# Optimization experiments

Hardware: AMD Instinct MI355X
Metric: run time of the kernel (lower is better)

## Reference

```python
import jax, jax.numpy as jnp
import numpy as np

N, E, R = 30000, 480000, 8192
N_IN, E_IN = 128, 64
N_HID, E_HID = 256, 128
N_OUT, E_OUT = 256, 64
N_CLASS, N_COL = 10, 128
NEG = 0.01  # LeakyReLU slope


def leaky(x):
    return jnp.where(x > 0, x, NEG * x)


def pe_init(n_pos, d):
    # sinusoid position encoding table (position_encoding_init)
    pe = np.array([[p / np.power(10000, 2 * (j // 2) / d) for j in range(d)]
                   if p != 0 else np.zeros(d) for p in range(n_pos)])
    pe[1:, 0::2] = np.sin(pe[1:, 0::2])
    pe[1:, 1::2] = np.cos(pe[1:, 1::2])
    return jnp.asarray(pe, jnp.float32)


def segment_mean(vals, idx, n):
    s = jax.ops.segment_sum(vals, idx, num_segments=n)
    c = jax.ops.segment_sum(jnp.ones((vals.shape[0], 1), vals.dtype), idx, num_segments=n)
    return s / jnp.maximum(c, 1.0)


def esage(x, e, src, dst, We, be, Wn, bn):
    # edge update from [x_src ; e], mean-aggregate messages to dst nodes, node update
    e2 = leaky(jnp.concatenate([x[src], e], axis=-1) @ We + be)      # [E, e_out]
    h = segment_mean(e2, dst, x.shape[0])                             # [N, e_out]
    x2 = leaky(jnp.concatenate([x, h], axis=-1) @ Wn + bn)            # [N, n_out]
    return x2, e2


def setup_inputs():
    key = jax.random.key(0)
    ks = jax.random.split(key, 24)

    def xav(k, shp):
        std = float(np.sqrt(2.0 / (shp[0] + shp[1])))
        return jax.random.normal(k, shp, jnp.float32) * std

    return {
        'x': jax.random.normal(ks[0], (N, N_IN), jnp.float32),
        'e': jax.random.normal(ks[1], (E, E_IN), jnp.float32),
        'src': jax.random.randint(ks[2], (E,), 0, N),
        'dst': jax.random.randint(ks[3], (E,), 0, N),
        'row_idx': jax.random.randint(ks[4], (R,), 0, N),
        'col_idx': jax.random.randint(ks[5], (N_COL,), 0, N),
        'real': jax.random.normal(ks[6], (R * N_COL, E_OUT), jnp.float32),
        'mask': jax.random.randint(ks[7], (R, N_COL), 0, 2) == 1,
        'W1e': xav(ks[8], (N_IN + E_IN, E_HID)), 'b1e': jnp.zeros((E_HID,), jnp.float32),
        'W1n': xav(ks[9], (N_IN + E_HID, N_HID)), 'b1n': jnp.zeros((N_HID,), jnp.float32),
        'W2e': xav(ks[10], (N_HID + E_HID, E_OUT)), 'b2e': jnp.zeros((E_OUT,), jnp.float32),
        'W2n': xav(ks[11], (N_HID + E_OUT, N_OUT)), 'b2n': jnp.zeros((N_OUT,), jnp.float32),
        'node_pe': pe_init(N_COL, N_HID),
        'Wq': xav(ks[12], (N_HID, N_HID)),
        'Wk': xav(ks[13], (N_HID, N_HID)),
        'Wv': xav(ks[14], (N_HID, N_HID)),
        'Wref': xav(ks[15], (N_HID, N_HID)), 'bref': jnp.zeros((N_HID,), jnp.float32),
        'Wr': xav(ks[16], (N_OUT, E_OUT)),
        'Wc': xav(ks[17], (N_HID, E_OUT)), 'bep': jnp.zeros((E_OUT,), jnp.float32),
        'Wcls': xav(ks[18], (N_COL * E_OUT, N_CLASS)), 'bcls': jnp.zeros((N_CLASS,), jnp.float32),
    }


def reference(x, e, src, dst, row_idx, col_idx, real, mask,
              W1e, b1e, W1n, b1n, W2e, b2e, W2n, b2n,
              node_pe, Wq, Wk, Wv, Wref, bref, Wr, Wc, bep, Wcls, bcls):
    # two ESAGE message-passing layers
    x1, e1 = esage(x, e, src, dst, W1e, b1e, W1n, b1n)
    new_col = x1[col_idx]                                  # [C, n_hidden]
    x2, e2 = esage(x1, e1, src, dst, W2e, b2e, W2n, b2n)
    new_row = x2[row_idx]                                  # [R, n_out]

    # node self-attention (hand-rolled, incl. the duplicated dist@v from the source)
    c = new_col + node_pe
    q, k, v = c @ Wq, c @ Wk, c @ Wv
    dist = jax.nn.softmax((q @ k.T) * (1.0 / np.sqrt(N_HID)), axis=-1)
    c = 2.0 * (dist @ v)                                    # mm(dist,v) + mm(dist,v)
    new_col = jax.nn.sigmoid(c @ Wref + bref)

    # edge predictor over all (row, col) pairs: [R, C, e_out]
    pred = leaky((new_row @ Wr)[:, None, :] + (new_col @ Wc)[None, :, :] + bep)
    pred_flat = pred.reshape(R * N_COL, E_OUT)

    # masked imputation: real where mask True, predicted elsewhere
    imput_e = jnp.where(mask.reshape(-1)[:, None], real, pred_flat)
    imput_e = imput_e.reshape(R, N_COL, E_OUT)

    # mlp classifier: Flatten -> Linear -> LogSoftmax
    res = jax.nn.log_softmax(imput_e.reshape(R, -1) @ Wcls + bcls, axis=-1)
    return (res, pred_flat)
```

## Files before the change

### kernel.cpp

```cpp
#include <hip/hip_runtime.h>
#include <hip/hip_bf16.h>
#include <math.h>

#define NNODES 30000
#define NEDGES 480000
#define RROWS  8192
#define NCOLS  128
#define NIN    128
#define EIN    64
#define NHID   256
#define EHID   128
#define NOUTD  256
#define EOUTD  64
#define NCLS   10
#define NB_PFX 118

typedef __attribute__((ext_vector_type(8))) unsigned short ushort8;
typedef __attribute__((ext_vector_type(8))) short bhalf8;
typedef __attribute__((ext_vector_type(4))) float floatx4;

__device__ __forceinline__ float lrelu(float v){ return v > 0.f ? v : 0.01f * v; }
__device__ __forceinline__ float4 ld4(const float* p){ return *(const float4*)p; }
__device__ __forceinline__ float4 ntld4(const float* p){
    floatx4 v = __builtin_nontemporal_load((const floatx4*)p);
    return make_float4(v.x, v.y, v.z, v.w);
}
__device__ __forceinline__ void ntst4(float* p, float4 v){
    floatx4 n = {v.x, v.y, v.z, v.w};
    __builtin_nontemporal_store(n, (floatx4*)p);
}
__device__ __forceinline__ void ntst8u(unsigned short* p, ushort8 v){
    __builtin_nontemporal_store(v, (ushort8*)p);
}
__device__ __forceinline__ unsigned short f2b(float f){
    unsigned int u = __builtin_bit_cast(unsigned int, f);
    u += 0x7fffu + ((u >> 16) & 1u);
    return (unsigned short)(u >> 16);
}
__device__ __forceinline__ float b2f(unsigned short b){
    unsigned int u = ((unsigned int)b) << 16;
    return __builtin_bit_cast(float, u);
}

#define PREP_CVT_N   1875
#define PREP_W1T_B   (PREP_CVT_N)
#define PREP_W1B_B   (PREP_W1T_B + 64)
#define PREP_W2T_B   (PREP_W1B_B + 32)
#define PREP_W2B_B   (PREP_W2T_B + 64)
#define PREP_W1N_B   (PREP_W2B_B + 32)
#define PREP_W2N_B   (PREP_W1N_B + 256)
#define PREP_HIST_B  (PREP_W2N_B + 320)
#define PREP_DET_B   (PREP_HIST_B + 1875)
#define PREP_TOTAL   (PREP_DET_B + 1)

__device__ __forceinline__ void wT_region(const float* __restrict__ W, unsigned short* __restrict__ Wt,
                                          int KOFF, int KSUB, int N, int idx){
    if (idx >= N * KSUB) return;
    int n = idx / KSUB, k = idx % KSUB;
    Wt[idx] = f2b(W[(size_t)(KOFF + k) * N + n]);
}

__global__ __launch_bounds__(256) void k_prep(
    const float* __restrict__ x, unsigned short* __restrict__ xb,
    const float* __restrict__ W1e, unsigned short* __restrict__ W1tT, unsigned short* __restrict__ W1bT,
    const float* __restrict__ W2e, unsigned short* __restrict__ W2tT, unsigned short* __restrict__ W2bT,
    const float* __restrict__ W1n, unsigned short* __restrict__ W1nTb,
    const float* __restrict__ W2n, unsigned short* __restrict__ W2nTb,
    const int* __restrict__ dst, int* __restrict__ cnt_i,
    const unsigned int* __restrict__ mask, int* __restrict__ mode)
{
    const int bid = blockIdx.x, t = threadIdx.x;
    if (bid < PREP_CVT_N){
        int i = bid * 256 + t;
        float4 a = ntld4(x + (size_t)i * 8), b = ntld4(x + (size_t)i * 8 + 4);
        ushort8 o = {f2b(a.x), f2b(a.y), f2b(a.z), f2b(a.w), f2b(b.x), f2b(b.y), f2b(b.z), f2b(b.w)};
        *(ushort8*)(xb + (size_t)i * 8) = o;
    } else if (bid < PREP_W1B_B){
        wT_region(W1e, W1tT, 0, 128, 128, (bid - PREP_W1T_B) * 256 + t);
    } else if (bid < PREP_W2T_B){
        wT_region(W1e, W1bT, 128, 64, 128, (bid - PREP_W1B_B) * 256 + t);
    } else if (bid < PREP_W2B_B){
        wT_region(W2e, W2tT, 0, 256, 64, (bid - PREP_W2T_B) * 256 + t);
    } else if (bid < PREP_W1N_B){
        wT_region(W2e, W2bT, 256, 128, 64, (bid - PREP_W2B_B) * 256 + t);
    } else if (bid < PREP_W2N_B){
        wT_region(W1n, W1nTb, 0, 256, 256, (bid - PREP_W1N_B) * 256 + t);
    } else if (bid < PREP_HIST_B){
        wT_region(W2n, W2nTb, 0, 320, 256, (bid - PREP_W2N_B) * 256 + t);
    } else if (bid < PREP_DET_B){
        int i = (bid - PREP_HIST_B) * 256 + t;
        if (i < NEDGES) atomicAdd(&cnt_i[dst[i]], 1);
    } else if (t == 0){
        bool allI32 = true, allF32 = true;
        for (int i = 0; i < 64; i++){
            unsigned int v = mask[i];
            if (!(v == 0u || v == 1u)) allI32 = false;
            if (!(v == 0u || v == 0x3F800000u)) allF32 = false;
        }
        *mode = allI32 ? 0 : (allF32 ? 1 : 2);
    }
}

__global__ __launch_bounds__(256) void k_pfx1(const int* __restrict__ cnt_i, int* __restrict__ blocksum){
    __shared__ int red[256];
    const int t = threadIdx.x;
    const int i = blockIdx.x * 256 + t;
    red[t] = (i < NNODES) ? cnt_i[i] : 0;
    __syncthreads();
    for (int o = 128; o; o >>= 1){ if (t < o) red[t] += red[t + o]; __syncthreads(); }
    if (t == 0) blocksum[blockIdx.x] = red[0];
}
__global__ __launch_bounds__(128) void k_pfx2(const int* __restrict__ blocksum, int* __restrict__ blockoff){
    __shared__ int s[128];
    const int t = threadIdx.x;
    int v = (t < NB_PFX) ? blocksum[t] : 0;
    s[t] = v;
    __syncthreads();
    for (int o = 1; o < 128; o <<= 1){
        int add = (t >= o) ? s[t - o] : 0;
        __syncthreads();
        s[t] += add;
        __syncthreads();
    }
    if (t < NB_PFX) blockoff[t] = s[t] - v;
}
__global__ __launch_bounds__(256) void k_pfx3(const int* __restrict__ cnt_i, const int* __restrict__ blockoff,
                                              int* __restrict__ cursor, float* __restrict__ cntf){
    __shared__ int s[256];
    const int t = threadIdx.x;
    const int i = blockIdx.x * 256 + t;
    int v = (i < NNODES) ? cnt_i[i] : 0;
    s[t] = v;
    __syncthreads();
    for (int o = 1; o < 256; o <<= 1){
        int add = (t >= o) ? s[t - o] : 0;
        __syncthreads();
        s[t] += add;
        __syncthreads();
    }
    if (i < NNODES){
        cursor[i] = s[t] - v + blockoff[blockIdx.x];
        cntf[i] = (float)v;
    }
}

__global__ void k_scatter(const int* __restrict__ dst, int* __restrict__ cursor, int* __restrict__ eidx){
    int i = blockIdx.x * 256 + threadIdx.x;
    if (i >= NEDGES) return;
    int pos = atomicAdd(&cursor[dst[i]], 1);
    eidx[pos] = i;
}
__global__ void k_sgather(const int* __restrict__ src, const int* __restrict__ dst,
                          const int* __restrict__ eidx,
                          int* __restrict__ srcs, int* __restrict__ dsts){
    int p = blockIdx.x * 256 + threadIdx.x;
    if (p >= NEDGES) return;
    int i = eidx[p];
    srcs[p] = src[i];
    dsts[p] = dst[i];
}

template<int K, int N>
__global__ __launch_bounds__(256) void k_gemm_b16(
    const unsigned short* __restrict__ Ab, const unsigned short* __restrict__ Wt,
    unsigned short* __restrict__ outb, int M)
{
    __shared__ unsigned short At[64][K + 8];
    const int t = threadIdx.x;
    const int r0 = blockIdx.x * 64;
    {
        const int r = t >> 2, q = t & 3;
        const int row = r0 + r;
        const bool valid = row < M;
        const unsigned short* a = Ab + (size_t)(valid ? row : 0) * K;
        for (int kk = q * (K / 4); kk < (q + 1) * (K / 4); kk += 8){
            ushort8 u;
            if (valid) u = *(const ushort8*)(a + kk);
            else       u = (ushort8){0,0,0,0,0,0,0,0};
            *(ushort8*)&At[r][kk] = u;
        }
    }
    __syncthreads();
    const int lane = t & 63, w = t >> 6;
    const int fr = lane & 15, fq = lane >> 4;
    constexpr int NF = N / 16;
    floatx4 acc[NF] = {};
    #pragma unroll
    for (int ks = 0; ks < K / 32; ks++){
        const int k = ks * 32 + fq * 8;
        bhalf8 a = *(bhalf8*)&At[w * 16 + fr][k];
        #pragma unroll
        for (int n = 0; n < NF; n++){
            bhalf8 b = *(const bhalf8*)(Wt + (size_t)(n * 16 + fr) * K + k);
            acc[n] = __builtin_amdgcn_mfma_f32_16x16x32_bf16(a, b, acc[n], 0, 0, 0);
        }
    }
    #pragma unroll
    for (int n = 0; n < NF; n++){
        const int col = n * 16 + fr;
        #pragma unroll
        for (int rr = 0; rr < 4; rr++){
            const int row = r0 + w * 16 + fq * 4 + rr;
            if (row < M) outb[(size_t)row * N + col] = f2b(acc[n][rr]);
        }
    }
}

__global__ __launch_bounds__(256) void k_edge1_fused(
    const float* __restrict__ e,
    const int* __restrict__ srcs, const int* __restrict__ dsts, const int* __restrict__ eidx,
    const unsigned short* __restrict__ W1bT, const float* __restrict__ b1e,
    const unsigned short* __restrict__ P1b, const unsigned short* __restrict__ W2bT,
    unsigned short* __restrict__ Qb, float* __restrict__ hsum)
{
    __shared__ unsigned short Cb[64][136];
    __shared__ unsigned short P1s[64][136];
    __shared__ int dstS[64];
    const int t = threadIdx.x;
    const int r = t >> 2, q = t & 3;
    const int lane = t & 63, w = t >> 6;
    const int wm = w >> 1, wn = w & 1;
    const int fr = lane & 15, fq = lane >> 4;
    const int base = blockIdx.x * 128;

    float4 f0, f1, f2, f3;
    ushort8 u0, u1, u2, u3;
    int dcur;

    {
        const int p = base + r;
        dcur = dsts[p];
        const int srow = srcs[p];
        const int ei = eidx[p];
        const float* ep = e + (size_t)ei * 64 + q * 16;
        f0 = ntld4(ep); f1 = ntld4(ep + 4); f2 = ntld4(ep + 8); f3 = ntld4(ep + 12);
        const unsigned short* pp = P1b + (size_t)srow * 128 + q * 32;
        u0 = *(const ushort8*)pp;       u1 = *(const ushort8*)(pp + 8);
        u2 = *(const ushort8*)(pp + 16); u3 = *(const ushort8*)(pp + 24);
    }

    #pragma unroll
    for (int tile = 0; tile < 2; tile++){
        const int p0 = base + tile * 64;
        if (tile) __syncthreads();
        if (q == 0) dstS[r] = dcur;
        {
            ushort8 e0 = {f2b(f0.x), f2b(f0.y), f2b(f0.z), f2b(f0.w), f2b(f1.x), f2b(f1.y), f2b(f1.z), f2b(f1.w)};
            ushort8 e1v = {f2b(f2.x), f2b(f2.y), f2b(f2.z), f2b(f2.w), f2b(f3.x), f2b(f3.y), f2b(f3.z), f2b(f3.w)};
            *(ushort8*)&Cb[r][q * 16]     = e0;
            *(ushort8*)&Cb[r][q * 16 + 8] = e1v;
            *(ushort8*)&P1s[r][q * 32]      = u0;
            *(ushort8*)&P1s[r][q * 32 + 8]  = u1;
            *(ushort8*)&P1s[r][q * 32 + 16] = u2;
            *(ushort8*)&P1s[r][q * 32 + 24] = u3;
        }
        __syncthreads();
        if (tile == 0){
            const int p = base + 64 + r;
            dcur = dsts[p];
            const int srow = srcs[p];
            const int ei = eidx[p];
            const float* ep = e + (size_t)ei * 64 + q * 16;
            f0 = ntld4(ep); f1 = ntld4(ep + 4); f2 = ntld4(ep + 8); f3 = ntld4(ep + 12);
            const unsigned short* pp = P1b + (size_t)srow * 128 + q * 32;
            u0 = *(const ushort8*)pp;       u1 = *(const ushort8*)(pp + 8);
            u2 = *(const ushort8*)(pp + 16); u3 = *(const ushort8*)(pp + 24);
        }
        floatx4 acc1[2][4] = {};
        #pragma unroll
        for (int ks = 0; ks < 2; ks++){
            const int k = ks * 32 + fq * 8;
            bhalf8 a0 = *(bhalf8*)&Cb[wm * 32 + fr][k];
            bhalf8 a1 = *(bhalf8*)&Cb[wm * 32 + 16 + fr][k];
            #pragma unroll
            for (int n = 0; n < 4; n++){
                const int col = wn * 64 + n * 16 + fr;
                bhalf8 b = *(const bhalf8*)(W1bT + (size_t)col * 64 + k);
                acc1[0][n] = __builtin_amdgcn_mfma_f32_16x16x32_bf16(a0, b, acc1[0][n], 0, 0, 0);
                acc1[1][n] = __builtin_amdgcn_mfma_f32_16x16x32_bf16(a1, b, acc1[1][n], 0, 0, 0);
            }
        }
        __syncthreads();
        #pragma unroll
        for (int m = 0; m < 2; m++){
            #pragma unroll
            for (int n = 0; n < 4; n++){
                const int col = wn * 64 + n * 16 + fr;
                const float bv = b1e[col];
                #pragma unroll
                for (int rr = 0; rr < 4; rr++){
                    const int row = wm * 32 + m * 16 + fq * 4 + rr;
                    const float pv = b2f(P1s[row][col]);
                    Cb[row][col] = f2b(lrelu(acc1[m][n][rr] + pv + bv));
                }
            }
        }
        __syncthreads();
        {
            floatx4 acc2[4] = {};
            #pragma unroll
            for (int ks = 0; ks < 4; ks++){
                const int k = ks * 32 + fq * 8;
                bhalf8 a = *(bhalf8*)&Cb[w * 16 + fr][k];
                #pragma unroll
                for (int n = 0; n < 4; n++){
                    bhalf8 b = *(const bhalf8*)(W2bT + (size_t)(n * 16 + fr) * 128 + k);
                    acc2[n] = __builtin_amdgcn_mfma_f32_16x16x32_bf16(a, b, acc2[n], 0, 0, 0);
                }
            }
            #pragma unroll
            for (int n = 0; n < 4; n++){
                const int col = n * 16 + fr;
                #pragma unroll
                for (int rr = 0; rr < 4; rr++){
                    const int row = w * 16 + fq * 4 + rr;
                    P1s[row][col] = f2b(acc2[n][rr]);
                }
            }
        }
        __syncthreads();
        {
            unsigned short* op = Qb + (size_t)(p0 + r) * 64 + q * 16;
            ntst8u(op,     *(ushort8*)&P1s[r][q * 16]);
            ntst8u(op + 8, *(ushort8*)&P1s[r][q * 16 + 8]);
        }
        {
            const int col = t & 127, half = t >> 7;
            const int rbase = half * 32;
            float s = 0.f;
            int prev = dstS[rbase];
            #pragma unroll 4
            for (int rr = 0; rr < 32; rr++){
                const int rw2 = rbase + rr;
                const int d = dstS[rw2];
                if (d != prev){
                    atomicAdd(&hsum[(size_t)prev * EHID + col], s);
                    s = 0.f; prev = d;
                }
                s += b2f(Cb[rw2][col]);
            }
            atomicAdd(&hsum[(size_t)prev * EHID + col], s);
        }
    }
}

__global__ __launch_bounds__(256) void k_edge2_lite(
    const unsigned short* __restrict__ P2b, const unsigned short* __restrict__ Qb,
    const int* __restrict__ srcs, const int* __restrict__ dsts,
    const float* __restrict__ b2e, float* __restrict__ hsum)
{
    const int t = threadIdx.x;
    const int lane = t & 63, w = t >> 6;
    const int p0 = blockIdx.x * 256 + w * 64;
    const float bias = b2e[lane];
    float s = 0.f;
    int prev = dsts[p0];
    #pragma unroll 4
    for (int i = 0; i < 64; i++){
        const int p = p0 + i;
        const int d = dsts[p];
        if (d != prev){
            atomicAdd(&hsum[(size_t)prev * EOUTD + lane], s);
            s = 0.f; prev = d;
        }
        const float q  = b2f(__builtin_nontemporal_load(&Qb[(size_t)p * 64 + lane]));
        const float pv = b2f(P2b[(size_t)srcs[p] * 64 + lane]);
        s += lrelu(pv + q + bias);
    }
    atomicAdd(&hsum[(size_t)prev * EOUTD + lane], s);
}

__global__ __launch_bounds__(256) void k_node1_p2(
    const unsigned short* __restrict__ A1b, const float* __restrict__ hsum,
    const float* __restrict__ cntf,
    const unsigned short* __restrict__ Wt, const float* __restrict__ bias,
    const unsigned short* __restrict__ W2tT,
    unsigned short* __restrict__ x1b, unsigned short* __restrict__ P2b, int M)
{
    constexpr int K = 256;
    __shared__ unsigned short At[32][K + 8];
    const int t = threadIdx.x;
    const int r0 = blockIdx.x * 32;
    {
        const int r = t >> 3, q = t & 7;
        const int row = r0 + r;
        const bool valid = row < M;
        float rinv = 0.f;
        const unsigned short* a1 = A1b;
        const float* a2 = hsum;
        if (valid){
            rinv = 1.f / fmaxf(cntf[row], 1.f);
            a1 = A1b  + (size_t)row * NIN;
            a2 = hsum + (size_t)row * EHID;
        }
        for (int kk = q * 32; kk < q * 32 + 32; kk += 8){
            ushort8 u;
            if (!valid){
                u = (ushort8){0,0,0,0,0,0,0,0};
            } else if (kk < NIN){
                u = *(const ushort8*)(a1 + kk);
            } else {
                float4 g0 = ld4(a2 + (kk - NIN)), g1 = ld4(a2 + (kk - NIN) + 4);
                u = (ushort8){f2b(g0.x*rinv), f2b(g0.y*rinv), f2b(g0.z*rinv), f2b(g0.w*rinv),
                              f2b(g1.x*rinv), f2b(g1.y*rinv), f2b(g1.z*rinv), f2b(g1.w*rinv)};
            }
            *(ushort8*)&At[r][kk] = u;
        }
    }
    __syncthreads();
    const int lane = t & 63, w = t >> 6;
    const int wm = w >> 1, wn = w & 1;
    const int fr = lane & 15, fq = lane >> 4;
    floatx4 acc[8] = {};
    #pragma unroll
    for (int ks = 0; ks < 8; ks++){
        const int k = ks * 32 + fq * 8;
        bhalf8 a = *(bhalf8*)&At[wm * 16 + fr][k];
        #pragma unroll
        for (int n = 0; n < 8; n++){
            const int col = wn * 128 + n * 16 + fr;
            bhalf8 b = *(const bhalf8*)(Wt + (size_t)col * K + k);
            acc[n] = __builtin_amdgcn_mfma_f32_16x16x32_bf16(a, b, acc[n], 0, 0, 0);
        }
    }
    __syncthreads();
    #pragma unroll
    for (int n = 0; n < 8; n++){
        const int col = wn * 128 + n * 16 + fr;
        const float bv = bias[col];
        #pragma unroll
        for (int rr = 0; rr < 4; rr++){
            const int row = r0 + wm * 16 + fq * 4 + rr;
            unsigned short ob = f2b(lrelu(acc[n][rr] + bv));
            At[wm * 16 + fq * 4 + rr][col] = ob;
            if (row < M) x1b[(size_t)row * 256 + col] = ob;
        }
    }
    __syncthreads();
    {
        floatx4 acc2[2] = {};
        #pragma unroll
        for (int ks = 0; ks < 8; ks++){
            const int k = ks * 32 + fq * 8;
            bhalf8 a = *(bhalf8*)&At[wm * 16 + fr][k];
            #pragma unroll
            for (int n = 0; n < 2; n++){
                const int col = wn * 32 + n * 16 + fr;
                bhalf8 b = *(const bhalf8*)(W2tT + (size_t)col * 256 + k);
                acc2[n] = __builtin_amdgcn_mfma_f32_16x16x32_bf16(a, b, acc2[n], 0, 0, 0);
            }
        }
        #pragma unroll
        for (int n = 0; n < 2; n++){
            const int col = wn * 32 + n * 16 + fr;
            #pragma unroll
            for (int rr = 0; rr < 4; rr++){
                const int row = r0 + wm * 16 + fq * 4 + rr;
                if (row < M) P2b[(size_t)row * 64 + col] = f2b(acc2[n][rr]);
            }
        }
    }
}

__global__ __launch_bounds__(256) void k_node2(
    const unsigned short* __restrict__ A1b, const float* __restrict__ hsum,
    const float* __restrict__ cntf,
    const unsigned short* __restrict__ Wt, const float* __restrict__ bias,
    unsigned short* __restrict__ outb, int M)
{
    constexpr int K = 320;
    __shared__ unsigned short At[32][K + 8];
    const int t = threadIdx.x;
    const int r0 = blockIdx.x * 32;
    {
        const int r = t >> 3, q = t & 7;
        const int row = r0 + r;
        const bool valid = row < M;
        float rinv = 0.f;
        const unsigned short* a1 = A1b;
        const float* a2 = hsum;
        if (valid){
            rinv = 1.f / fmaxf(cntf[row], 1.f);
            a1 = A1b  + (size_t)row * NHID;
            a2 = hsum + (size_t)row * EOUTD;
        }
        for (int kk = q * 40; kk < q * 40 + 40; kk += 8){
            ushort8 u;
            if (!valid){
                u = (ushort8){0,0,0,0,0,0,0,0};
            } else if (kk < NHID){
                u = *(const ushort8*)(a1 + kk);
            } else {
                float4 g0 = ld4(a2 + (kk - NHID)), g1 = ld4(a2 + (kk - NHID) + 4);
                u = (ushort8){f2b(g0.x*rinv), f2b(g0.y*rinv), f2b(g0.z*rinv), f2b(g0.w*rinv),
                              f2b(g1.x*rinv), f2b(g1.y*rinv), f2b(g1.z*rinv), f2b(g1.w*rinv)};
            }
            *(ushort8*)&At[r][kk] = u;
        }
    }
    __syncthreads();
    const int lane = t & 63, w = t >> 6;
    const int wm = w >> 1, wn = w & 1;
    const int fr = lane & 15, fq = lane >> 4;
    floatx4 acc[8] = {};
    #pragma unroll
    for (int ks = 0; ks < 10; ks++){
        const int k = ks * 32 + fq * 8;
        bhalf8 a = *(bhalf8*)&At[wm * 16 + fr][k];
        #pragma unroll
        for (int n = 0; n < 8; n++){
            const int col = wn * 128 + n * 16 + fr;
            bhalf8 b = *(const bhalf8*)(Wt + (size_t)col * K + k);
            acc[n] = __builtin_amdgcn_mfma_f32_16x16x32_bf16(a, b, acc[n], 0, 0, 0);
        }
    }
    #pragma unroll
    for (int n = 0; n < 8; n++){
        const int col = wn * 128 + n * 16 + fr;
        const float bv = bias[col];
        #pragma unroll
        for (int rr = 0; rr < 4; rr++){
            const int row = r0 + wm * 16 + fq * 4 + rr;
            if (row < M) outb[(size_t)row * 256 + col] = f2b(lrelu(acc[n][rr] + bv));
        }
    }
}

__global__ __launch_bounds__(256) void k_attn_qkv(
    const unsigned short* __restrict__ x1b, const int* __restrict__ col_idx,
    const float* __restrict__ pe,
    const float* __restrict__ Wq, const float* __restrict__ Wk, const float* __restrict__ Wv,
    float* __restrict__ qo, float* __restrict__ ko, float* __restrict__ vo)
{
    __shared__ float c[256];
    const int i = blockIdx.x, t = threadIdx.x;
    const int col = col_idx[i];
    c[t] = b2f(x1b[(size_t)col * 256 + t]) + pe[i * 256 + t];
    __syncthreads();
    float aq = 0.f, ak = 0.f, av = 0.f;
    #pragma unroll 4
    for (int kk = 0; kk < 256; kk++){
        float cv = c[kk];
        aq += cv * Wq[kk * 256 + t];
        ak += cv * Wk[kk * 256 + t];
        av += cv * Wv[kk * 256 + t];
    }
    qo[i * 256 + t] = aq; ko[i * 256 + t] = ak; vo[i * 256 + t] = av;
}

__global__ __launch_bounds__(128) void k_attn_dist(
    const float* __restrict__ q, const float* __restrict__ k, float* __restrict__ dist)
{
    __shared__ float qr[256];
    __shared__ float red[128];
    const int i = blockIdx.x, t = threadIdx.x;
    qr[t] = q[i * 256 + t]; qr[t + 128] = q[i * 256 + t + 128];
    __syncthreads();
    float s = 0.f;
    #pragma unroll 4
    for (int kk = 0; kk < 256; kk++) s += qr[kk] * k[t * 256 + kk];
    s *= 0.0625f;
    red[t] = s; __syncthreads();
    for (int off = 64; off; off >>= 1){ if (t < off) red[t] = fmaxf(red[t], red[t + off]); __syncthreads(); }
    float m = red[0]; __syncthreads();
    float ex = expf(s - m);
    red[t] = ex; __syncthreads();
    for (int off = 64; off; off >>= 1){ if (t < off) red[t] += red[t + off]; __syncthreads(); }
    dist[i * 128 + t] = ex / red[0];
}

__global__ __launch_bounds__(256) void k_attn_out(
    const float* __restrict__ dist, const float* __restrict__ v,
    const float* __restrict__ Wref, const float* __restrict__ bref,
    const float* __restrict__ Wc, const float* __restrict__ bep,
    float* __restrict__ colWc)
{
    __shared__ float dr[128];
    __shared__ float c2[256];
    __shared__ float nc[256];
    const int i = blockIdx.x, t = threadIdx.x;
    if (t < 128) dr[t] = dist[i * 128 + t];
    __syncthreads();
    float s = 0.f;
    #pragma unroll 4
    for (int j = 0; j < 128; j++) s += dr[j] * v[j * 256 + t];
    c2[t] = 2.f * s;
    __syncthreads();
    float a = 0.f;
    #pragma unroll 4
    for (int kk = 0; kk < 256; kk++) a += c2[kk] * Wref[kk * 256 + t];
    a += bref[t];
    nc[t] = 1.f / (1.f + expf(-a));
    __syncthreads();
    if (t < 64){
        float o = 0.f;
        #pragma unroll 4
        for (int kk = 0; kk < 256; kk++) o += nc[kk] * Wc[kk * 64 + t];
        colWc[i * 64 + t] = o + bep[t];
    }
}

__global__ __launch_bounds__(256) void k_rowwr(
    const unsigned short* __restrict__ x2b, const int* __restrict__ row_idx,
    const float* __restrict__ Wr, float* __restrict__ rw)
{
    __shared__ unsigned short A[16][264];
    const int t = threadIdx.x;
    const int r0 = blockIdx.x * 16;
    const int rl = t >> 4, cg = t & 15;
    const int ridx = row_idx[r0 + rl];
    const unsigned short* ar = x2b + (size_t)ridx * 256;
    for (int i = cg; i < 32; i += 16) *(ushort8*)&A[rl][i * 8] = *(const ushort8*)(ar + i * 8);
    __syncthreads();
    float acc[4] = {0.f, 0.f, 0.f, 0.f};
    #pragma unroll 4
    for (int kk = 0; kk < 256; kk++){
        float4 w = ld4(Wr + (size_t)kk * 64 + cg * 4);
        float a = b2f(A[rl][kk]);
        acc[0] += a * w.x; acc[1] += a * w.y; acc[2] += a * w.z; acc[3] += a * w.w;
    }
    *(float4*)(rw + (size_t)(r0 + rl) * 64 + cg * 4) = make_float4(acc[0], acc[1], acc[2], acc[3]);
}

__global__ __launch_bounds__(256) void k_pred8(
    const float* __restrict__ rowWr, const float* __restrict__ colWc,
    const void* __restrict__ maskp, const int* __restrict__ modep,
    const float* __restrict__ real, const float* __restrict__ Wcls, const float* __restrict__ bcls,
    float* __restrict__ out)
{
    __shared__ float colWc_s[8192];
    __shared__ float rowWr_s[8 * 64];
    __shared__ unsigned char mask_s[8 * 128];
    __shared__ float part[4][80];
    __shared__ float logits_s[80];
    const int t  = threadIdx.x;
    const int r0 = blockIdx.x * 8;
    const int mode = *modep;
    for (int idx = t; idx < 2048; idx += 256)
        *(float4*)&colWc_s[idx * 4] = ld4(colWc + idx * 4);
    for (int idx = t; idx < 128; idx += 256)
        *(float4*)&rowWr_s[idx * 4] = ld4(rowWr + (size_t)r0 * 64 + idx * 4);
    for (int idx = t; idx < 1024; idx += 256){
        const int g = idx >> 7, c = idx & 127;
        const int gi = (r0 + g) * 128 + c;
        bool m;
        if (mode == 2)      m = ((const unsigned char*)maskp)[gi] != 0;
        else if (mode == 0) m = ((const int*)maskp)[gi] != 0;
        else                m = ((const float*)maskp)[gi] != 0.f;
        mask_s[idx] = m ? 1 : 0;
    }
    __syncthreads();

    float acc[8][10];
    #pragma unroll
    for (int g = 0; g < 8; g++)
        #pragma unroll
        for (int c = 0; c < 10; c++) acc[g][c] = 0.f;
    float* pred = out + RROWS * NCLS;

    #pragma unroll 1
    for (int i = 0; i < 8; i++){
        const int e4   = i * 256 + t;
        const int base = e4 * 4;
        const int c = base >> 6;
        const int j = base & 63;
        float4 cw = ld4(&colWc_s[c * 64 + j]);
        float w40[40];
        #pragma unroll
        for (int u = 0; u < 10; u++){
            float4 wv = ld4(Wcls + (size_t)base * 10 + u * 4);
            w40[u*4+0] = wv.x; w40[u*4+1] = wv.y; w40[u*4+2] = wv.z; w40[u*4+3] = wv.w;
        }
        #pragma unroll
        for (int g = 0; g < 8; g++){
            const int rr = r0 + g;
            float4 rwv = ld4(&rowWr_s[g * 64 + j]);
            float4 p;
            p.x = lrelu(rwv.x + cw.x); p.y = lrelu(rwv.y + cw.y);
            p.z = lrelu(rwv.z + cw.z); p.w = lrelu(rwv.w + cw.w);
            ntst4(pred + (size_t)rr * 8192 + base, p);
            float4 im = p;
            if (mask_s[g * 128 + c]) im = ntld4(real + (size_t)rr * 8192 + base);
            #pragma unroll
            for (int cls = 0; cls < 10; cls++){
                acc[g][cls] += im.x * w40[cls]      + im.y * w40[10 + cls]
                             + im.z * w40[20 + cls] + im.w * w40[30 + cls];
            }
        }
    }
    #pragma unroll
    for (int g = 0; g < 8; g++)
        #pragma unroll
        for (int cls = 0; cls < 10; cls++){
            float v = acc[g][cls];
            for (int off = 32; off; off >>= 1) v += __shfl_down(v, off, 64);
            acc[g][cls] = v;
        }
    const int wid = t >> 6, lane = t & 63;
    if (lane == 0){
        #pragma unroll
        for (int g = 0; g < 8; g++)
            #pragma unroll
            for (int cls = 0; cls < 10; cls++) part[wid][g * 10 + cls] = acc[g][cls];
    }
    __syncthreads();
    if (t < 80) logits_s[t] = part[0][t] + part[1][t] + part[2][t] + part[3][t] + bcls[t % 10];
    __syncthreads();
    if (t < 8){
        float m = -1e30f;
        #pragma unroll
        for (int cls = 0; cls < 10; cls++) m = fmaxf(m, logits_s[t * 10 + cls]);
        float se = 0.f;
        #pragma unroll
        for (int cls = 0; cls < 10; cls++) se += expf(logits_s[t * 10 + cls] - m);
        float ls = logf(se) + m;
        #pragma unroll
        for (int cls = 0; cls < 10; cls++) out[(r0 + t) * 10 + cls] = logits_s[t * 10 + cls] - ls;
    }
}

extern "C" void kernel_launch(void* const* d_in, const int* in_sizes, int n_in,
                              void* d_out, int out_size, void* d_ws, size_t ws_size,
                              hipStream_t stream)
{
    const float* x      = (const float*)d_in[0];
    const float* e      = (const float*)d_in[1];
    const int*   src    = (const int*)d_in[2];
    const int*   dst    = (const int*)d_in[3];
    const int*   row_idx= (const int*)d_in[4];
    const int*   col_idx= (const int*)d_in[5];
    const float* real   = (const float*)d_in[6];
    const void*  mask   = d_in[7];
    const float* W1e    = (const float*)d_in[8];
    const float* b1e    = (const float*)d_in[9];
    const float* W1n    = (const float*)d_in[10];
    const float* b1n    = (const float*)d_in[11];
    const float* W2e    = (const float*)d_in[12];
    const float* b2e    = (const float*)d_in[13];
    const float* W2n    = (const float*)d_in[14];
    const float* b2n    = (const float*)d_in[15];
    const float* pe     = (const float*)d_in[16];
    const float* Wq     = (const float*)d_in[17];
    const float* Wk     = (const float*)d_in[18];
    const float* Wv     = (const float*)d_in[19];
    const float* Wref   = (const float*)d_in[20];
    const float* bref   = (const float*)d_in[21];
    const float* Wr     = (const float*)d_in[22];
    const float* Wc     = (const float*)d_in[23];
    const float* bep    = (const float*)d_in[24];
    const float* Wcls   = (const float*)d_in[25];
    const float* bcls   = (const float*)d_in[26];

    float* ws = (float*)d_ws;
    size_t off = 0;
    float* h1sum = ws + off; off += (size_t)NNODES * EHID;
    float* h2sum = ws + off; off += (size_t)NNODES * EOUTD;
    int*   cnt_i = (int*)(ws + off); off += NNODES;
    const size_t zero_floats = off;
    float* cntf  = ws + off; off += NNODES;
    int*   cursor= (int*)(ws + off); off += NNODES;
    int*   srcs  = (int*)(ws + off); off += NEDGES;
    int*   dsts  = (int*)(ws + off); off += NEDGES;
    int*   eidx  = (int*)(ws + off); off += NEDGES;
    unsigned short* xb    = (unsigned short*)(ws + off); off += (size_t)NNODES * NIN  / 2;
    unsigned short* x1b   = (unsigned short*)(ws + off); off += (size_t)NNODES * NHID / 2;
    unsigned short* x2b   = (unsigned short*)(ws + off); off += (size_t)NNODES * NOUTD / 2;
    unsigned short* W1tT  = (unsigned short*)(ws + off); off += 128 * 128 / 2;
    unsigned short* W1bT  = (unsigned short*)(ws + off); off += 128 * 64 / 2;
    unsigned short* W2tT  = (unsigned short*)(ws + off); off += 64 * 256 / 2;
    unsigned short* W2bT  = (unsigned short*)(ws + off); off += 64 * 128 / 2;
    unsigned short* W1nTb = (unsigned short*)(ws + off); off += 256 * 256 / 2;
    unsigned short* W2nTb = (unsigned short*)(ws + off); off += 256 * 320 / 2;
    unsigned short* P1b   = (unsigned short*)(ws + off); off += (size_t)NNODES * 128 / 2;
    unsigned short* P2b   = (unsigned short*)(ws + off); off += (size_t)NNODES * 64 / 2;
    float* qb    = ws + off; off += 128 * 256;
    float* kb    = ws + off; off += 128 * 256;
    float* vb    = ws + off; off += 128 * 256;
    float* distb = ws + off; off += 128 * 128;
    float* colWc = ws + off; off += 128 * 64;
    float* rowWrb= ws + off; off += (size_t)RROWS * EOUTD;
    int*   modep = (int*)(ws + off); off += 4;
    int*   blocksum = (int*)(ws + off); off += 128;
    int*   blockoff = (int*)(ws + off); off += 128;
    unsigned short* Qb;
    size_t need = (off + (size_t)NEDGES * 32) * sizeof(float);
    if (ws_size >= need) Qb = (unsigned short*)(ws + off);
    else                 Qb = (unsigned short*)((float*)d_out + (size_t)RROWS * NCLS);

    (void)hipMemsetAsync(d_ws, 0, zero_floats * sizeof(float), stream);
    k_prep<<<PREP_TOTAL, 256, 0, stream>>>(x, xb, W1e, W1tT, W1bT, W2e, W2tT, W2bT,
                                           W1n, W1nTb, W2n, W2nTb, dst, cnt_i,
                                           (const unsigned int*)mask, modep);
    k_pfx1<<<NB_PFX, 256, 0, stream>>>(cnt_i, blocksum);
    k_pfx2<<<1, 128, 0, stream>>>(blocksum, blockoff);
    k_pfx3<<<NB_PFX, 256, 0, stream>>>(cnt_i, blockoff, cursor, cntf);
    k_scatter<<<(NEDGES + 255) / 256, 256, 0, stream>>>(dst, cursor, eidx);
    k_sgather<<<(NEDGES + 255) / 256, 256, 0, stream>>>(src, dst, eidx, srcs, dsts);
    k_gemm_b16<128, 128><<<(NNODES + 63) / 64, 256, 0, stream>>>(xb, W1tT, P1b, NNODES);
    k_edge1_fused<<<NEDGES / 128, 256, 0, stream>>>(e, srcs, dsts, eidx, W1bT, b1e, P1b, W2bT, Qb, h1sum);
    k_node1_p2<<<(NNODES + 31) / 32, 256, 0, stream>>>(xb, h1sum, cntf, W1nTb, b1n, W2tT, x1b, P2b, NNODES);
    k_edge2_lite<<<NEDGES / 256, 256, 0, stream>>>(P2b, Qb, srcs, dsts, b2e, h2sum);
    k_node2<<<(NNODES + 31) / 32, 256, 0, stream>>>(x1b, h2sum, cntf, W2nTb, b2n, x2b, NNODES);
    k_attn_qkv<<<128, 256, 0, stream>>>(x1b, col_idx, pe, Wq, Wk, Wv, qb, kb, vb);
    k_attn_dist<<<128, 128, 0, stream>>>(qb, kb, distb);
    k_attn_out<<<128, 256, 0, stream>>>(distb, vb, Wref, bref, Wc, bep, colWc);
    k_rowwr<<<RROWS / 16, 256, 0, stream>>>(x2b, row_idx, Wr, rowWrb);
    k_pred8<<<RROWS / 8, 256, 0, stream>>>(rowWrb, colWc, mask, modep, real, Wcls, bcls, (float*)d_out);
}
```

Before: 627.1 us.

## Pre-gather edge features to sorted bf16 buffer in sgather; simplify edge1 kernel

```diff
diff --git a/kernel.cpp b/kernel.cpp
--- a/kernel.cpp
+++ b/kernel.cpp
@@ -150,14 +150,23 @@
     int pos = atomicAdd(&cursor[dst[i]], 1);
     eidx[pos] = i;
 }
-__global__ void k_sgather(const int* __restrict__ src, const int* __restrict__ dst,
-                          const int* __restrict__ eidx,
-                          int* __restrict__ srcs, int* __restrict__ dsts){
-    int p = blockIdx.x * 256 + threadIdx.x;
-    if (p >= NEDGES) return;
-    int i = eidx[p];
-    srcs[p] = src[i];
-    dsts[p] = dst[i];
+
+__global__ __launch_bounds__(256) void k_sgather(
+    const int* __restrict__ src, const int* __restrict__ dst, const int* __restrict__ eidx,
+    const float* __restrict__ e,
+    int* __restrict__ srcs, int* __restrict__ dsts, unsigned short* __restrict__ es)
+{
+    const int t = threadIdx.x;
+    const int r = t >> 2, q = t & 3;
+    const int p = blockIdx.x * 64 + r;
+    const int i = eidx[p];
+    if (q == 0){ srcs[p] = src[i]; dsts[p] = dst[i]; }
+    const float* ep = e + (size_t)i * 64 + q * 16;
+    float4 f0 = ntld4(ep), f1 = ntld4(ep + 4), f2 = ntld4(ep + 8), f3 = ntld4(ep + 12);
+    ushort8 u0 = {f2b(f0.x), f2b(f0.y), f2b(f0.z), f2b(f0.w), f2b(f1.x), f2b(f1.y), f2b(f1.z), f2b(f1.w)};
+    ushort8 u1 = {f2b(f2.x), f2b(f2.y), f2b(f2.z), f2b(f2.w), f2b(f3.x), f2b(f3.y), f2b(f3.z), f2b(f3.w)};
+    ntst8u(es + (size_t)p * 64 + q * 16,     u0);
+    ntst8u(es + (size_t)p * 64 + q * 16 + 8, u1);
 }
 
 template<int K, int N>
@@ -207,8 +216,8 @@
 }
 
 __global__ __launch_bounds__(256) void k_edge1_fused(
-    const float* __restrict__ e,
-    const int* __restrict__ srcs, const int* __restrict__ dsts, const int* __restrict__ eidx,
+    const unsigned short* __restrict__ es,
+    const int* __restrict__ srcs, const int* __restrict__ dsts,
     const unsigned short* __restrict__ W1bT, const float* __restrict__ b1e,
     const unsigned short* __restrict__ P1b, const unsigned short* __restrict__ W2bT,
     unsigned short* __restrict__ Qb, float* __restrict__ hsum)
@@ -217,130 +226,99 @@
     __shared__ unsigned short P1s[64][136];
     __shared__ int dstS[64];
     const int t = threadIdx.x;
+    const int p0 = blockIdx.x * 64;
     const int r = t >> 2, q = t & 3;
+    {
+        const int p = p0 + r;
+        if (q == 0) dstS[r] = dsts[p];
+        const int srow = srcs[p];
+        const unsigned short* pp = P1b + (size_t)srow * 128 + q * 32;
+        *(ushort8*)&P1s[r][q * 32]      = *(const ushort8*)pp;
+        *(ushort8*)&P1s[r][q * 32 + 8]  = *(const ushort8*)(pp + 8);
+        *(ushort8*)&P1s[r][q * 32 + 16] = *(const ushort8*)(pp + 16);
+        *(ushort8*)&P1s[r][q * 32 + 24] = *(const ushort8*)(pp + 24);
+        const unsigned short* ep = es + (size_t)p * 64 + q * 16;
+        *(ushort8*)&Cb[r][q * 16]     = *(const ushort8*)ep;
+        *(ushort8*)&Cb[r][q * 16 + 8] = *(const ushort8*)(ep + 8);
+    }
+    __syncthreads();
     const int lane = t & 63, w = t >> 6;
     const int wm = w >> 1, wn = w & 1;
     const int fr = lane & 15, fq = lane >> 4;
-    const int base = blockIdx.x * 128;
-
-    float4 f0, f1, f2, f3;
-    ushort8 u0, u1, u2, u3;
-    int dcur;
-
-    {
-        const int p = base + r;
-        dcur = dsts[p];
-        const int srow = srcs[p];
-        const int ei = eidx[p];
-        const float* ep = e + (size_t)ei * 64 + q * 16;
-        f0 = ntld4(ep); f1 = ntld4(ep + 4); f2 = ntld4(ep + 8); f3 = ntld4(ep + 12);
-        const unsigned short* pp = P1b + (size_t)srow * 128 + q * 32;
-        u0 = *(const ushort8*)pp;       u1 = *(const ushort8*)(pp + 8);
-        u2 = *(const ushort8*)(pp + 16); u3 = *(const ushort8*)(pp + 24);
-    }
-
-    #pragma unroll
-    for (int tile = 0; tile < 2; tile++){
-        const int p0 = base + tile * 64;
-        if (tile) __syncthreads();
-        if (q == 0) dstS[r] = dcur;
-        {
-            ushort8 e0 = {f2b(f0.x), f2b(f0.y), f2b(f0.z), f2b(f0.w), f2b(f1.x), f2b(f1.y), f2b(f1.z), f2b(f1.w)};
-            ushort8 e1v = {f2b(f2.x), f2b(f2.y), f2b(f2.z), f2b(f2.w), f2b(f3.x), f2b(f3.y), f2b(f3.z), f2b(f3.w)};
-            *(ushort8*)&Cb[r][q * 16]     = e0;
-            *(ushort8*)&Cb[r][q * 16 + 8] = e1v;
-            *(ushort8*)&P1s[r][q * 32]      = u0;
-            *(ushort8*)&P1s[r][q * 32 + 8]  = u1;
-            *(ushort8*)&P1s[r][q * 32 + 16] = u2;
-            *(ushort8*)&P1s[r][q * 32 + 24] = u3;
-        }
-        __syncthreads();
-        if (tile == 0){
-            const int p = base + 64 + r;
-            dcur = dsts[p];
-            const int srow = srcs[p];
-            const int ei = eidx[p];
-            const float* ep = e + (size_t)ei * 64 + q * 16;
-            f0 = ntld4(ep); f1 = ntld4(ep + 4); f2 = ntld4(ep + 8); f3 = ntld4(ep + 12);
-            const unsigned short* pp = P1b + (size_t)srow * 128 + q * 32;
-            u0 = *(const ushort8*)pp;       u1 = *(const ushort8*)(pp + 8);
-            u2 = *(const ushort8*)(pp + 16); u3 = *(const ushort8*)(pp + 24);
-        }
-        floatx4 acc1[2][4] = {};
-        #pragma unroll
-        for (int ks = 0; ks < 2; ks++){
+    floatx4 acc1[2][4] = {};
+    #pragma unroll
+    for (int ks = 0; ks < 2; ks++){
+        const int k = ks * 32 + fq * 8;
+        bhalf8 a0 = *(bhalf8*)&Cb[wm * 32 + fr][k];
+        bhalf8 a1 = *(bhalf8*)&Cb[wm * 32 + 16 + fr][k];
+        #pragma unroll
+        for (int n = 0; n < 4; n++){
+            const int col = wn * 64 + n * 16 + fr;
+            bhalf8 b = *(const bhalf8*)(W1bT + (size_t)col * 64 + k);
+            acc1[0][n] = __builtin_amdgcn_mfma_f32_16x16x32_bf16(a0, b, acc1[0][n], 0, 0, 0);
+            acc1[1][n] = __builtin_amdgcn_mfma_f32_16x16x32_bf16(a1, b, acc1[1][n], 0, 0, 0);
+        }
+    }
+    __syncthreads();
+    #pragma unroll
+    for (int m = 0; m < 2; m++){
+        #pragma unroll
+        for (int n = 0; n < 4; n++){
+            const int col = wn * 64 + n * 16 + fr;
+            const float bv = b1e[col];
+            #pragma unroll
+            for (int rr = 0; rr < 4; rr++){
+                const int row = wm * 32 + m * 16 + fq * 4 + rr;
+                const float pv = b2f(P1s[row][col]);
+                Cb[row][col] = f2b(lrelu(acc1[m][n][rr] + pv + bv));
+            }
+        }
+    }
+    __syncthreads();
+    {
+        floatx4 acc2[4] = {};
+        #pragma unroll
+        for (int ks = 0; ks < 4; ks++){
             const int k = ks * 32 + fq * 8;
-            bhalf8 a0 = *(bhalf8*)&Cb[wm * 32 + fr][k];
-            bhalf8 a1 = *(bhalf8*)&Cb[wm * 32 + 16 + fr][k];
+            bhalf8 a = *(bhalf8*)&Cb[w * 16 + fr][k];
             #pragma unroll
             for (int n = 0; n < 4; n++){
-                const int col = wn * 64 + n * 16 + fr;
-                bhalf8 b = *(const bhalf8*)(W1bT + (size_t)col * 64 + k);
-                acc1[0][n] = __builtin_amdgcn_mfma_f32_16x16x32_bf16(a0, b, acc1[0][n], 0, 0, 0);
-                acc1[1][n] = __builtin_amdgcn_mfma_f32_16x16x32_bf16(a1, b, acc1[1][n], 0, 0, 0);
-            }
-        }
-        __syncthreads();
-        #pragma unroll
-        for (int m = 0; m < 2; m++){
+                bhalf8 b = *(const bhalf8*)(W2bT + (size_t)(n * 16 + fr) * 128 + k);
+                acc2[n] = __builtin_amdgcn_mfma_f32_16x16x32_bf16(a, b, acc2[n], 0, 0, 0);
+            }
+        }
+        #pragma unroll
+        for (int n = 0; n < 4; n++){
+            const int col = n * 16 + fr;
             #pragma unroll
-            for (int n = 0; n < 4; n++){
-                const int col = wn * 64 + n * 16 + fr;
-                const float bv = b1e[col];
-                #pragma unroll
-                for (int rr = 0; rr < 4; rr++){
-                    const int row = wm * 32 + m * 16 + fq * 4 + rr;
-                    const float pv = b2f(P1s[row][col]);
-                    Cb[row][col] = f2b(lrelu(acc1[m][n][rr] + pv + bv));
-                }
-            }
-        }
-        __syncthreads();
-        {
-            floatx4 acc2[4] = {};
-            #pragma unroll
-            for (int ks = 0; ks < 4; ks++){
-                const int k = ks * 32 + fq * 8;
-                bhalf8 a = *(bhalf8*)&Cb[w * 16 + fr][k];
-                #pragma unroll
-                for (int n = 0; n < 4; n++){
-                    bhalf8 b = *(const bhalf8*)(W2bT + (size_t)(n * 16 + fr) * 128 + k);
-                    acc2[n] = __builtin_amdgcn_mfma_f32_16x16x32_bf16(a, b, acc2[n], 0, 0, 0);
-                }
-            }
-            #pragma unroll
-            for (int n = 0; n < 4; n++){
-                const int col = n * 16 + fr;
-                #pragma unroll
-                for (int rr = 0; rr < 4; rr++){
-                    const int row = w * 16 + fq * 4 + rr;
-                    P1s[row][col] = f2b(acc2[n][rr]);
-                }
-            }
-        }
-        __syncthreads();
-        {
-            unsigned short* op = Qb + (size_t)(p0 + r) * 64 + q * 16;
-            ntst8u(op,     *(ushort8*)&P1s[r][q * 16]);
-            ntst8u(op + 8, *(ushort8*)&P1s[r][q * 16 + 8]);
-        }
-        {
-            const int col = t & 127, half = t >> 7;
-            const int rbase = half * 32;
-            float s = 0.f;
-            int prev = dstS[rbase];
-            #pragma unroll 4
-            for (int rr = 0; rr < 32; rr++){
-                const int rw2 = rbase + rr;
-                const int d = dstS[rw2];
-                if (d != prev){
-                    atomicAdd(&hsum[(size_t)prev * EHID + col], s);
-                    s = 0.f; prev = d;
-                }
-                s += b2f(Cb[rw2][col]);
-            }
-            atomicAdd(&hsum[(size_t)prev * EHID + col], s);
-        }
+            for (int rr = 0; rr < 4; rr++){
+                const int row = w * 16 + fq * 4 + rr;
+                P1s[row][col] = f2b(acc2[n][rr]);
+            }
+        }
+    }
+    __syncthreads();
+    {
+        unsigned short* op = Qb + (size_t)(p0 + r) * 64 + q * 16;
+        ntst8u(op,     *(ushort8*)&P1s[r][q * 16]);
+        ntst8u(op + 8, *(ushort8*)&P1s[r][q * 16 + 8]);
+    }
+    {
+        const int col = t & 127, half = t >> 7;
+        const int rbase = half * 32;
+        float s = 0.f;
+        int prev = dstS[rbase];
+        #pragma unroll 4
+        for (int rr = 0; rr < 32; rr++){
+            const int rw2 = rbase + rr;
+            const int d = dstS[rw2];
+            if (d != prev){
+                atomicAdd(&hsum[(size_t)prev * EHID + col], s);
+                s = 0.f; prev = d;
+            }
+            s += b2f(Cb[rw2][col]);
+        }
+        atomicAdd(&hsum[(size_t)prev * EHID + col], s);
     }
 }
 
@@ -782,10 +760,16 @@
     int*   modep = (int*)(ws + off); off += 4;
     int*   blocksum = (int*)(ws + off); off += 128;
     int*   blockoff = (int*)(ws + off); off += 128;
+    unsigned short* es;
     unsigned short* Qb;
-    size_t need = (off + (size_t)NEDGES * 32) * sizeof(float);
-    if (ws_size >= need) Qb = (unsigned short*)(ws + off);
-    else                 Qb = (unsigned short*)((float*)d_out + (size_t)RROWS * NCLS);
+    {
+        size_t need_es = (off + (size_t)NEDGES * 32) * sizeof(float);
+        if (ws_size >= need_es){ es = (unsigned short*)(ws + off); off += (size_t)NEDGES * 32; }
+        else                     es = (unsigned short*)((float*)d_out + (size_t)RROWS * NCLS + 20000000);
+        size_t need_q = (off + (size_t)NEDGES * 32) * sizeof(float);
+        if (ws_size >= need_q){ Qb = (unsigned short*)(ws + off); off += (size_t)NEDGES * 32; }
+        else                    Qb = (unsigned short*)((float*)d_out + (size_t)RROWS * NCLS);
+    }
 
     (void)hipMemsetAsync(d_ws, 0, zero_floats * sizeof(float), stream);
     k_prep<<<PREP_TOTAL, 256, 0, stream>>>(x, xb, W1e, W1tT, W1bT, W2e, W2tT, W2bT,
@@ -795,9 +779,9 @@
     k_pfx2<<<1, 128, 0, stream>>>(blocksum, blockoff);
     k_pfx3<<<NB_PFX, 256, 0, stream>>>(cnt_i, blockoff, cursor, cntf);
     k_scatter<<<(NEDGES + 255) / 256, 256, 0, stream>>>(dst, cursor, eidx);
-    k_sgather<<<(NEDGES + 255) / 256, 256, 0, stream>>>(src, dst, eidx, srcs, dsts);
+    k_sgather<<<NEDGES / 64, 256, 0, stream>>>(src, dst, eidx, e, srcs, dsts, es);
     k_gemm_b16<128, 128><<<(NNODES + 63) / 64, 256, 0, stream>>>(xb, W1tT, P1b, NNODES);
-    k_edge1_fused<<<NEDGES / 128, 256, 0, stream>>>(e, srcs, dsts, eidx, W1bT, b1e, P1b, W2bT, Qb, h1sum);
+    k_edge1_fused<<<NEDGES / 64, 256, 0, stream>>>(es, srcs, dsts, W1bT, b1e, P1b, W2bT, Qb, h1sum);
     k_node1_p2<<<(NNODES + 31) / 32, 256, 0, stream>>>(xb, h1sum, cntf, W1nTb, b1n, W2tT, x1b, P2b, NNODES);
     k_edge2_lite<<<NEDGES / 256, 256, 0, stream>>>(P2b, Qb, srcs, dsts, b2e, h2sum);
     k_node2<<<(NNODES + 31) / 32, 256, 0, stream>>>(x1b, h2sum, cntf, W2nTb, b2n, x2b, NNODES);
```

Result: no change. 625.0 us (-0.3%).
